# Performance work log

Hardware: AMD Instinct MI355X
Metric: run time of the kernel (lower is better)

The kernel has to match this reference:

```python
import jax, jax.numpy as jnp
import numpy as np

TOP_K = 2  # matches init kwarg top_k


def setup_inputs() -> dict:
    key = jax.random.key(0)
    k1, k2, k3, k4 = jax.random.split(key, 4)
    B, S, D, E = 4, 2048, 1024, 8
    x = jax.random.normal(k1, (B, S, D), dtype=jnp.float32)
    w_gate = jax.random.normal(k2, (D, E), dtype=jnp.float32) * 0.02
    w1 = jax.random.normal(k3, (E, D, 4 * D), dtype=jnp.float32) * 0.02
    w2 = jax.random.normal(k4, (E, 4 * D, D), dtype=jnp.float32) * 0.02
    return {"x": x, "w_gate": w_gate, "w1": w1, "w2": w2}


def reference(x, w_gate, w1, w2):
    # x: [B, S, D]; w_gate: [D, E]; w1: [E, D, 4D]; w2: [E, 4D, D]
    B, S, D = x.shape
    E = w1.shape[0]
    xt = x.reshape(-1, D)                      # [T, D], T = B*S
    T = xt.shape[0]

    logits = xt @ w_gate                       # [T, E]
    topk_vals, topk_idx = jax.lax.top_k(logits, TOP_K)  # [T, K]
    gates = jax.nn.softmax(topk_vals, axis=-1)          # [T, K]

    # Combine weights per (token, expert): scatter the top-k gates.
    comb = jnp.zeros((T, E), dtype=x.dtype)
    comb = comb.at[jnp.arange(T)[:, None], topk_idx].add(gates)  # [T, E]

    # Dense per-expert FFN over all tokens, masked by combine weight.
    # (Loop over the small fixed expert count; each iteration is a big GEMM.)
    out = jnp.zeros_like(xt)
    for e in range(E):
        h = jax.nn.relu(xt @ w1[e])            # [T, 4D]
        y = h @ w2[e]                          # [T, D]
        out = out + comb[:, e:e + 1] * y
    return out.reshape(B, S, D)
```

## Files before the change

### kernel.cpp

```cpp
#include <hip/hip_runtime.h>
#include <hip/hip_bf16.h>


#define T_TOK   8192
#define DIM     1024
#define NEXP    8
#define HID     4096

typedef unsigned short ushort_t;
typedef __attribute__((ext_vector_type(8))) short bfrag;
typedef __attribute__((ext_vector_type(4))) float f32x4;

__device__ __forceinline__ ushort_t f2bf(float f) {
    union { float f; unsigned int u; } v; v.f = f;
    unsigned int r = v.u + 0x7FFFu + ((v.u >> 16) & 1u);
    return (ushort_t)(r >> 16);
}

__device__ __forceinline__ void async_load16(const void* g, void* l) {
    __builtin_amdgcn_global_load_lds(
        (const __attribute__((address_space(1))) unsigned int*)g,
        (__attribute__((address_space(3))) unsigned int*)l, 16, 0, 0);
}

__global__ __launch_bounds__(256)
void route_kern(const float* __restrict__ x, const float* __restrict__ wg,
                ushort_t* __restrict__ x_bf, int* __restrict__ topk,
                float* __restrict__ gates, int* __restrict__ counts)
{
    const int w = threadIdx.x >> 6, lane = threadIdx.x & 63;
    const int t = blockIdx.x * 4 + w;
    const float* xr = x + (size_t)t * DIM;
    float acc[8];
#pragma unroll
    for (int e = 0; e < 8; ++e) acc[e] = 0.f;

#pragma unroll
    for (int it = 0; it < 4; ++it) {
        const int j = it * 256 + lane * 4;
        float4 xv = *(const float4*)(xr + j);
        ushort4 xb;
        xb.x = f2bf(xv.x); xb.y = f2bf(xv.y); xb.z = f2bf(xv.z); xb.w = f2bf(xv.w);
        *(ushort4*)(x_bf + (size_t)t * DIM + j) = xb;
        const float xs[4] = {xv.x, xv.y, xv.z, xv.w};
#pragma unroll
        for (int jj = 0; jj < 4; ++jj) {
            float4 g0 = *(const float4*)(wg + (size_t)(j + jj) * 8);
            float4 g1 = *(const float4*)(wg + (size_t)(j + jj) * 8 + 4);
            acc[0] += xs[jj] * g0.x; acc[1] += xs[jj] * g0.y;
            acc[2] += xs[jj] * g0.z; acc[3] += xs[jj] * g0.w;
            acc[4] += xs[jj] * g1.x; acc[5] += xs[jj] * g1.y;
            acc[6] += xs[jj] * g1.z; acc[7] += xs[jj] * g1.w;
        }
    }
#pragma unroll
    for (int d = 1; d < 64; d <<= 1)
#pragma unroll
        for (int e = 0; e < 8; ++e) acc[e] += __shfl_xor(acc[e], d);

    if (lane == 0) {
        int i0 = 0; float v0 = acc[0];
#pragma unroll
        for (int e = 1; e < 8; ++e) if (acc[e] > v0) { v0 = acc[e]; i0 = e; }
        int i1 = -1; float v1 = -1e30f;
#pragma unroll
        for (int e = 0; e < 8; ++e) if (e != i0 && acc[e] > v1) { v1 = acc[e]; i1 = e; }
        float ex = __expf(v1 - v0);
        float inv = 1.f / (1.f + ex);
        topk[t * 2] = i0; topk[t * 2 + 1] = i1;
        gates[t * 2] = inv; gates[t * 2 + 1] = ex * inv;
        atomicAdd(&counts[i0], 1);
        atomicAdd(&counts[i1], 1);
    }
}

__global__ void scan_kern(const int* __restrict__ counts, int* __restrict__ offs,
                          int* __restrict__ cursors)
{
    if (threadIdx.x == 0) {
        int o = 0;
        for (int e = 0; e < NEXP; ++e) { offs[e] = o; cursors[e] = o; o += counts[e]; }
        offs[NEXP] = o;
    }
}

__global__ __launch_bounds__(256)
void scatter_kern(const int* __restrict__ topk, const float* __restrict__ gates,
                  int* __restrict__ cursors, int* __restrict__ tok_c,
                  float* __restrict__ gate_c)
{
    const int t = blockIdx.x * 256 + threadIdx.x;
#pragma unroll
    for (int k = 0; k < 2; ++k) {
        int e = topk[t * 2 + k];
        int pos = atomicAdd(&cursors[e], 1);
        tok_c[pos] = t;
        gate_c[pos] = gates[t * 2 + k];
    }
}

__global__ __launch_bounds__(256)
void transp_kern(const float* __restrict__ in, ushort_t* __restrict__ out, int K, int N)
{
    __shared__ float tile[64][65];
    const int e = blockIdx.z;
    const size_t ibase = (size_t)e * K * N, obase = (size_t)e * N * K;
    const int k0 = blockIdx.y * 64, n0 = blockIdx.x * 64;
    const int tid = threadIdx.x;

    const int r = tid >> 4, c4 = (tid & 15) * 4;
#pragma unroll
    for (int p = 0; p < 4; ++p) {
        int kk = p * 16 + r;
        float4 v = *(const float4*)(in + ibase + (size_t)(k0 + kk) * N + n0 + c4);
        tile[kk][c4] = v.x; tile[kk][c4 + 1] = v.y; tile[kk][c4 + 2] = v.z; tile[kk][c4 + 3] = v.w;
    }
    __syncthreads();
    const int k8 = (tid & 7) * 8, nr = tid >> 3;
#pragma unroll
    for (int p = 0; p < 2; ++p) {
        int nn = p * 32 + nr;
        bfrag v;
#pragma unroll
        for (int j = 0; j < 8; ++j) v[j] = (short)f2bf(tile[k8 + j][nn]);
        *(bfrag*)(out + obase + (size_t)(n0 + nn) * K + k0 + k8) = v;
    }
}

template <int STAGE, int NTK, int SPLITK, int KF, int NF>
__global__ __launch_bounds__(256)
void gemm_kern(const ushort_t* __restrict__ A, const ushort_t* __restrict__ Bt,
               ushort_t* __restrict__ Hout, float* __restrict__ Out,
               const int* __restrict__ eoff, const int* __restrict__ tok_c,
               const float* __restrict__ gate_c)
{
    __shared__ ushort_t ldsA[128 * 64];
    __shared__ ushort_t ldsB[128 * 64];

    constexpr int NBN = NF / 128;
    const int e = blockIdx.z;
    const int base = eoff[e];
    const int cnt = eoff[e + 1] - base;
    const int m0 = blockIdx.y * 128;
    if (m0 >= cnt) return;
    const int nblk = blockIdx.x % NBN;
    const int ks = blockIdx.x / NBN;
    const int n0 = nblk * 128;
    const int kbeg = ks * NTK * 64;

    const int tid = threadIdx.x;
    const int w = tid >> 6, lane = tid & 63;
    const int lhi = lane >> 4, llo = lane & 15;

    const ushort_t* asrc[4];
    const ushort_t* bsrc[4];
    int ldsoff[4];
    const ushort_t* Bbase = Bt + (size_t)e * (size_t)NF * (size_t)KF;
#pragma unroll
    for (int i = 0; i < 4; ++i) {
        int ci = ((i * 4 + w) << 6) + lane;
        int r = ci >> 3;
        int cb = (ci & 7) << 4;
        int sb = cb ^ ((r & 7) << 4);
        int gr = m0 + r; if (gr >= cnt) gr = cnt - 1;
        size_t arow = (STAGE == 1) ? (size_t)tok_c[base + gr] * (size_t)KF
                                   : (size_t)(base + gr) * (size_t)KF;
        asrc[i] = A + arow + (sb >> 1);
        bsrc[i] = Bbase + (size_t)(n0 + r) * KF + (sb >> 1);
        ldsoff[i] = (i * 4 + w) << 10;
    }

    f32x4 acc[4][4];
#pragma unroll
    for (int m = 0; m < 4; ++m)
#pragma unroll
        for (int n = 0; n < 4; ++n) acc[m][n] = (f32x4)(0.f);

    const int wr = (w >> 1) << 6;
    const int wc = (w & 1) << 6;

    for (int kt = 0; kt < NTK; ++kt) {
        const int k0 = kbeg + kt * 64;
#pragma unroll
        for (int i = 0; i < 4; ++i) {
            async_load16(asrc[i] + k0, (char*)ldsA + ldsoff[i]);
            async_load16(bsrc[i] + k0, (char*)ldsB + ldsoff[i]);
        }
        __syncthreads();
#pragma unroll
        for (int s = 0; s < 2; ++s) {
            bfrag a[4], b[4];
            const int kb = (s << 6) + (lhi << 4);
#pragma unroll
            for (int m = 0; m < 4; ++m) {
                int row = wr + (m << 4) + llo;
                a[m] = *(const bfrag*)((const char*)ldsA + row * 128 + (kb ^ ((row & 7) << 4)));
            }
#pragma unroll
            for (int n = 0; n < 4; ++n) {
                int row = wc + (n << 4) + llo;
                b[n] = *(const bfrag*)((const char*)ldsB + row * 128 + (kb ^ ((row & 7) << 4)));
            }
#pragma unroll
            for (int m = 0; m < 4; ++m)
#pragma unroll
                for (int n = 0; n < 4; ++n)
                    acc[m][n] = __builtin_amdgcn_mfma_f32_16x16x32_bf16(a[m], b[n], acc[m][n], 0, 0, 0);
        }
        __syncthreads();
    }

    if (STAGE == 1) {
#pragma unroll
        for (int m = 0; m < 4; ++m)
#pragma unroll
            for (int i = 0; i < 4; ++i) {
                int row = wr + (m << 4) + (lhi << 2) + i;
                int gr = m0 + row;
                if (gr >= cnt) continue;
                size_t rb = (size_t)(base + gr) * (size_t)NF + n0 + wc;
#pragma unroll
                for (int n = 0; n < 4; ++n) {
                    float v = acc[m][n][i];
                    Hout[rb + (n << 4) + llo] = f2bf(v > 0.f ? v : 0.f);
                }
            }
    } else {
#pragma unroll
        for (int m = 0; m < 4; ++m)
#pragma unroll
            for (int i = 0; i < 4; ++i) {
                int row = wr + (m << 4) + (lhi << 2) + i;
                int gr = m0 + row;
                if (gr >= cnt) continue;
                int tok = tok_c[base + gr];
                float g = gate_c[base + gr];
                size_t rb = (size_t)tok * (size_t)NF + n0 + wc;
#pragma unroll
                for (int n = 0; n < 4; ++n)
                    atomicAdd(&Out[rb + (n << 4) + llo], g * acc[m][n][i]);
            }
    }
}

extern "C" void kernel_launch(void* const* d_in, const int* in_sizes, int n_in,
                              void* d_out, int out_size, void* d_ws, size_t ws_size,
                              hipStream_t stream)
{
    const float* x  = (const float*)d_in[0];
    const float* wg = (const float*)d_in[1];
    const float* w1 = (const float*)d_in[2];
    const float* w2 = (const float*)d_in[3];
    float* out = (float*)d_out;

    char* ws = (char*)d_ws;
    ushort_t* x_bf = (ushort_t*)(ws + 0);
    ushort_t* w1t  = (ushort_t*)(ws + 16777216);
    ushort_t* w2t  = (ushort_t*)(ws + 83886080);
    ushort_t* h    = (ushort_t*)(ws + 150994944);
    char* ctrl     = ws + 285212672;
    int*   topk    = (int*)(ctrl);
    float* gates   = (float*)(ctrl + 65536);
    int*   tok_c   = (int*)(ctrl + 131072);
    float* gate_c  = (float*)(ctrl + 196608);
    int*   counts  = (int*)(ctrl + 262144);
    int*   offs    = (int*)(ctrl + 262144 + 64);
    int*   cursors = (int*)(ctrl + 262144 + 128);

    hipMemsetAsync(counts, 0, NEXP * sizeof(int), stream);
    hipMemsetAsync(out, 0, (size_t)T_TOK * DIM * sizeof(float), stream);

    route_kern<<<T_TOK / 4, 256, 0, stream>>>(x, wg, x_bf, topk, gates, counts);
    transp_kern<<<dim3(HID / 64, DIM / 64, NEXP), 256, 0, stream>>>(w1, w1t, DIM, HID);
    transp_kern<<<dim3(DIM / 64, HID / 64, NEXP), 256, 0, stream>>>(w2, w2t, HID, DIM);
    scan_kern<<<1, 64, 0, stream>>>(counts, offs, cursors);
    scatter_kern<<<T_TOK / 256, 256, 0, stream>>>(topk, gates, cursors, tok_c, gate_c);

    gemm_kern<1, 16, 1, 1024, 4096><<<dim3(HID / 128, 64, NEXP), 256, 0, stream>>>(
        x_bf, w1t, h, nullptr, offs, tok_c, gate_c);
    gemm_kern<2, 32, 2, 4096, 1024><<<dim3((DIM / 128) * 2, 64, NEXP), 256, 0, stream>>>(
        h, w2t, nullptr, out, offs, tok_c, gate_c);
}
```

Measured before the change: 901.1 us.

## Enlarge GEMM tiles to 256x128 with 8 waves and drop split-K

The grouped expert GEMMs now use 512-thread blocks covering 256 rows by 128 columns, so each B tile loaded into LDS is shared by twice as many rows. Split-K for the second GEMM is removed, which halves the atomic adds to the output but doubles each block's K loop. Fewer, larger blocks may leave CUs idle for experts with few tokens, and more rows are wasted on partially filled M tiles.

Result: faster. 784.0 us (-13.0%).

```diff
diff --git a/kernel.cpp b/kernel.cpp
--- a/kernel.cpp
+++ b/kernel.cpp
@@ -127,47 +127,52 @@
     }
 }
 
-template <int STAGE, int NTK, int SPLITK, int KF, int NF>
-__global__ __launch_bounds__(256)
+template <int STAGE, int NTK, int KF, int NF>
+__global__ __launch_bounds__(512)
 void gemm_kern(const ushort_t* __restrict__ A, const ushort_t* __restrict__ Bt,
                ushort_t* __restrict__ Hout, float* __restrict__ Out,
                const int* __restrict__ eoff, const int* __restrict__ tok_c,
                const float* __restrict__ gate_c)
 {
-    __shared__ ushort_t ldsA[128 * 64];
+    __shared__ ushort_t ldsA[256 * 64];
     __shared__ ushort_t ldsB[128 * 64];
 
-    constexpr int NBN = NF / 128;
     const int e = blockIdx.z;
     const int base = eoff[e];
     const int cnt = eoff[e + 1] - base;
-    const int m0 = blockIdx.y * 128;
+    const int m0 = blockIdx.y * 256;
     if (m0 >= cnt) return;
-    const int nblk = blockIdx.x % NBN;
-    const int ks = blockIdx.x / NBN;
-    const int n0 = nblk * 128;
-    const int kbeg = ks * NTK * 64;
+    const int n0 = blockIdx.x * 128;
 
     const int tid = threadIdx.x;
     const int w = tid >> 6, lane = tid & 63;
     const int lhi = lane >> 4, llo = lane & 15;
+    const int wm = w >> 1;
+    const int wn = w & 1;
 
     const ushort_t* asrc[4];
-    const ushort_t* bsrc[4];
-    int ldsoff[4];
-    const ushort_t* Bbase = Bt + (size_t)e * (size_t)NF * (size_t)KF;
+    int aoff[4];
 #pragma unroll
     for (int i = 0; i < 4; ++i) {
-        int ci = ((i * 4 + w) << 6) + lane;
+        int ci = i * 512 + tid;
         int r = ci >> 3;
-        int cb = (ci & 7) << 4;
-        int sb = cb ^ ((r & 7) << 4);
+        int sb = (((ci & 7) ^ (r & 7)) << 4);
         int gr = m0 + r; if (gr >= cnt) gr = cnt - 1;
         size_t arow = (STAGE == 1) ? (size_t)tok_c[base + gr] * (size_t)KF
                                    : (size_t)(base + gr) * (size_t)KF;
         asrc[i] = A + arow + (sb >> 1);
+        aoff[i] = ci << 4;
+    }
+    const ushort_t* Bbase = Bt + (size_t)e * (size_t)NF * (size_t)KF;
+    const ushort_t* bsrc[2];
+    int boff[2];
+#pragma unroll
+    for (int i = 0; i < 2; ++i) {
+        int ci = i * 512 + tid;
+        int r = ci >> 3;
+        int sb = (((ci & 7) ^ (r & 7)) << 4);
         bsrc[i] = Bbase + (size_t)(n0 + r) * KF + (sb >> 1);
-        ldsoff[i] = (i * 4 + w) << 10;
+        boff[i] = ci << 4;
     }
 
     f32x4 acc[4][4];
@@ -176,16 +181,14 @@
 #pragma unroll
         for (int n = 0; n < 4; ++n) acc[m][n] = (f32x4)(0.f);
 
-    const int wr = (w >> 1) << 6;
-    const int wc = (w & 1) << 6;
-
     for (int kt = 0; kt < NTK; ++kt) {
-        const int k0 = kbeg + kt * 64;
-#pragma unroll
-        for (int i = 0; i < 4; ++i) {
-            async_load16(asrc[i] + k0, (char*)ldsA + ldsoff[i]);
-            async_load16(bsrc[i] + k0, (char*)ldsB + ldsoff[i]);
-        }
+        const int k0 = kt * 64;
+#pragma unroll
+        for (int i = 0; i < 4; ++i)
+            async_load16(asrc[i] + k0, (char*)ldsA + aoff[i]);
+#pragma unroll
+        for (int i = 0; i < 2; ++i)
+            async_load16(bsrc[i] + k0, (char*)ldsB + boff[i]);
         __syncthreads();
 #pragma unroll
         for (int s = 0; s < 2; ++s) {
@@ -193,12 +196,12 @@
             const int kb = (s << 6) + (lhi << 4);
 #pragma unroll
             for (int m = 0; m < 4; ++m) {
-                int row = wr + (m << 4) + llo;
+                int row = wm * 64 + (m << 4) + llo;
                 a[m] = *(const bfrag*)((const char*)ldsA + row * 128 + (kb ^ ((row & 7) << 4)));
             }
 #pragma unroll
             for (int n = 0; n < 4; ++n) {
-                int row = wc + (n << 4) + llo;
+                int row = wn * 64 + (n << 4) + llo;
                 b[n] = *(const bfrag*)((const char*)ldsB + row * 128 + (kb ^ ((row & 7) << 4)));
             }
 #pragma unroll
@@ -215,10 +218,10 @@
         for (int m = 0; m < 4; ++m)
 #pragma unroll
             for (int i = 0; i < 4; ++i) {
-                int row = wr + (m << 4) + (lhi << 2) + i;
+                int row = wm * 64 + (m << 4) + (lhi << 2) + i;
                 int gr = m0 + row;
                 if (gr >= cnt) continue;
-                size_t rb = (size_t)(base + gr) * (size_t)NF + n0 + wc;
+                size_t rb = (size_t)(base + gr) * (size_t)NF + n0 + wn * 64;
 #pragma unroll
                 for (int n = 0; n < 4; ++n) {
                     float v = acc[m][n][i];
@@ -230,12 +233,12 @@
         for (int m = 0; m < 4; ++m)
 #pragma unroll
             for (int i = 0; i < 4; ++i) {
-                int row = wr + (m << 4) + (lhi << 2) + i;
+                int row = wm * 64 + (m << 4) + (lhi << 2) + i;
                 int gr = m0 + row;
                 if (gr >= cnt) continue;
                 int tok = tok_c[base + gr];
                 float g = gate_c[base + gr];
-                size_t rb = (size_t)tok * (size_t)NF + n0 + wc;
+                size_t rb = (size_t)tok * (size_t)NF + n0 + wn * 64;
 #pragma unroll
                 for (int n = 0; n < 4; ++n)
                     atomicAdd(&Out[rb + (n << 4) + llo], g * acc[m][n][i]);
@@ -276,8 +279,8 @@
     scan_kern<<<1, 64, 0, stream>>>(counts, offs, cursors);
     scatter_kern<<<T_TOK / 256, 256, 0, stream>>>(topk, gates, cursors, tok_c, gate_c);
 
-    gemm_kern<1, 16, 1, 1024, 4096><<<dim3(HID / 128, 64, NEXP), 256, 0, stream>>>(
+    gemm_kern<1, 16, 1024, 4096><<<dim3(HID / 128, 32, NEXP), 512, 0, stream>>>(
         x_bf, w1t, h, nullptr, offs, tok_c, gate_c);
-    gemm_kern<2, 32, 2, 4096, 1024><<<dim3((DIM / 128) * 2, 64, NEXP), 256, 0, stream>>>(
+    gemm_kern<2, 64, 4096, 1024><<<dim3(DIM / 128, 32, NEXP), 512, 0, stream>>>(
         h, w2t, nullptr, out, offs, tok_c, gate_c);
 }
```

## Double-buffer LDS tiles in expert GEMM and drop split-K for second stage

Applied to the files above, without the earlier changes.

The grouped GEMM now holds two LDS buffers for A and B. It issues the async global-to-LDS loads for the next K tile before computing on the current one, using explicit vmcnt waits, raw barriers and raised wave priority around the MFMA section. The aim is to hide global load latency behind the matrix math. The second-stage GEMM no longer uses split-K and runs the full K range per block, which halves its grid and the number of accumulating writes into the output. In exchange, the doubled LDS footprint may lower occupancy, and stage 2 has less parallelism per expert.

Result: no change. 896.0 us (-0.6%).

```diff
diff --git a/kernel.cpp b/kernel.cpp
--- a/kernel.cpp
+++ b/kernel.cpp
@@ -127,26 +127,22 @@
     }
 }
 
-template <int STAGE, int NTK, int SPLITK, int KF, int NF>
+template <int STAGE, int NTK, int KF, int NF>
 __global__ __launch_bounds__(256)
 void gemm_kern(const ushort_t* __restrict__ A, const ushort_t* __restrict__ Bt,
                ushort_t* __restrict__ Hout, float* __restrict__ Out,
                const int* __restrict__ eoff, const int* __restrict__ tok_c,
                const float* __restrict__ gate_c)
 {
-    __shared__ ushort_t ldsA[128 * 64];
-    __shared__ ushort_t ldsB[128 * 64];
-
-    constexpr int NBN = NF / 128;
+    __shared__ ushort_t ldsA[2][128 * 64];
+    __shared__ ushort_t ldsB[2][128 * 64];
+
     const int e = blockIdx.z;
     const int base = eoff[e];
     const int cnt = eoff[e + 1] - base;
     const int m0 = blockIdx.y * 128;
     if (m0 >= cnt) return;
-    const int nblk = blockIdx.x % NBN;
-    const int ks = blockIdx.x / NBN;
-    const int n0 = nblk * 128;
-    const int kbeg = ks * NTK * 64;
+    const int n0 = blockIdx.x * 128;
 
     const int tid = threadIdx.x;
     const int w = tid >> 6, lane = tid & 63;
@@ -170,6 +166,15 @@
         ldsoff[i] = (i * 4 + w) << 10;
     }
 
+    auto stage = [&](int buf, int kt) {
+        const int k0 = kt * 64;
+#pragma unroll
+        for (int i = 0; i < 4; ++i) {
+            async_load16(asrc[i] + k0, (char*)(&ldsA[buf][0]) + ldsoff[i]);
+            async_load16(bsrc[i] + k0, (char*)(&ldsB[buf][0]) + ldsoff[i]);
+        }
+    };
+
     f32x4 acc[4][4];
 #pragma unroll
     for (int m = 0; m < 4; ++m)
@@ -179,14 +184,19 @@
     const int wr = (w >> 1) << 6;
     const int wc = (w & 1) << 6;
 
+    stage(0, 0);
+    int cur = 0;
     for (int kt = 0; kt < NTK; ++kt) {
-        const int k0 = kbeg + kt * 64;
-#pragma unroll
-        for (int i = 0; i < 4; ++i) {
-            async_load16(asrc[i] + k0, (char*)ldsA + ldsoff[i]);
-            async_load16(bsrc[i] + k0, (char*)ldsB + ldsoff[i]);
-        }
-        __syncthreads();
+        if (kt + 1 < NTK) {
+            stage(cur ^ 1, kt + 1);
+            asm volatile("s_waitcnt vmcnt(8)" ::: "memory");
+        } else {
+            asm volatile("s_waitcnt vmcnt(0)" ::: "memory");
+        }
+        __builtin_amdgcn_s_barrier();
+        const char* pA = (const char*)(&ldsA[cur][0]);
+        const char* pB = (const char*)(&ldsB[cur][0]);
+        __builtin_amdgcn_s_setprio(1);
 #pragma unroll
         for (int s = 0; s < 2; ++s) {
             bfrag a[4], b[4];
@@ -194,12 +204,12 @@
 #pragma unroll
             for (int m = 0; m < 4; ++m) {
                 int row = wr + (m << 4) + llo;
-                a[m] = *(const bfrag*)((const char*)ldsA + row * 128 + (kb ^ ((row & 7) << 4)));
+                a[m] = *(const bfrag*)(pA + row * 128 + (kb ^ ((row & 7) << 4)));
             }
 #pragma unroll
             for (int n = 0; n < 4; ++n) {
                 int row = wc + (n << 4) + llo;
-                b[n] = *(const bfrag*)((const char*)ldsB + row * 128 + (kb ^ ((row & 7) << 4)));
+                b[n] = *(const bfrag*)(pB + row * 128 + (kb ^ ((row & 7) << 4)));
             }
 #pragma unroll
             for (int m = 0; m < 4; ++m)
@@ -207,7 +217,9 @@
                 for (int n = 0; n < 4; ++n)
                     acc[m][n] = __builtin_amdgcn_mfma_f32_16x16x32_bf16(a[m], b[n], acc[m][n], 0, 0, 0);
         }
-        __syncthreads();
+        __builtin_amdgcn_s_setprio(0);
+        __builtin_amdgcn_s_barrier();
+        cur ^= 1;
     }
 
     if (STAGE == 1) {
@@ -276,8 +288,8 @@
     scan_kern<<<1, 64, 0, stream>>>(counts, offs, cursors);
     scatter_kern<<<T_TOK / 256, 256, 0, stream>>>(topk, gates, cursors, tok_c, gate_c);
 
-    gemm_kern<1, 16, 1, 1024, 4096><<<dim3(HID / 128, 64, NEXP), 256, 0, stream>>>(
+    gemm_kern<1, 16, 1024, 4096><<<dim3(HID / 128, 64, NEXP), 256, 0, stream>>>(
         x_bf, w1t, h, nullptr, offs, tok_c, gate_c);
-    gemm_kern<2, 32, 2, 4096, 1024><<<dim3((DIM / 128) * 2, 64, NEXP), 256, 0, stream>>>(
+    gemm_kern<2, 64, 4096, 1024><<<dim3(DIM / 128, 64, NEXP), 256, 0, stream>>>(
         h, w2t, nullptr, out, offs, tok_c, gate_c);
 }
```
